# Kernel optimization log

Hardware: AMD Instinct MI355X
Metric: run time of the kernel (lower is better)

The kernel has to match this reference:

```python
import jax, jax.numpy as jnp
import numpy as np

B, S, D, H, E, K = 2, 1024, 512, 2048, 64, 2
EPS = 1e-5


def setup_inputs() -> dict:
    key = jax.random.key(0)
    ks = jax.random.split(key, 5)
    s = 0.02  # small init scale for stability
    return {
        "x": jax.random.normal(ks[0], (B, S, D), dtype=jnp.float32),
        "Wg": jax.random.normal(ks[1], (D, E), dtype=jnp.float32) * s,
        "bg": jnp.zeros((E,), dtype=jnp.float32),
        "W1": jax.random.normal(ks[2], (E, D, H), dtype=jnp.float32) * s,
        "b1": jnp.zeros((E, H), dtype=jnp.float32),
        "W2": jax.random.normal(ks[3], (E, H, D), dtype=jnp.float32) * s,
        "b2": jnp.zeros((E, D), dtype=jnp.float32),
        "gamma": jnp.ones((D,), dtype=jnp.float32),
        "beta": jnp.zeros((D,), dtype=jnp.float32),
    }


def reference(x, Wg, bg, W1, b1, W2, b2, gamma, beta):
    # Gating: softmax over experts, keep top-k weights, zero the rest (scatter)
    probs = jax.nn.softmax(x @ Wg + bg, axis=-1)          # [B,S,E]
    topk_vals, topk_idx = jax.lax.top_k(probs, K)          # [B,S,K]
    sparse_w = jnp.sum(
        jax.nn.one_hot(topk_idx, E, dtype=probs.dtype) * topk_vals[..., None],
        axis=-2,
    )                                                      # [B,S,E]

    # Dense MoE: run every expert FFN on every token (faithful to source)
    h = jax.nn.relu(jnp.einsum('bsd,edh->bseh', x, W1) + b1)   # [B,S,E,H]
    expert_out = jnp.einsum('bseh,ehd->bsed', h, W2) + b2      # [B,S,E,D]

    # Weighted combine + residual
    out = jnp.einsum('bse,bsed->bsd', sparse_w, expert_out) + x

    # LayerNorm (eps=1e-5, elementwise affine)
    mu = out.mean(-1, keepdims=True)
    var = ((out - mu) ** 2).mean(-1, keepdims=True)
    return (out - mu) * jax.lax.rsqrt(var + EPS) * gamma + beta
```

## Files before the change

### kernel.cpp

```cpp
#include <hip/hip_runtime.h>
#include <hip/hip_bf16.h>

#define NTOK 2048
#define DIM 512
#define HID 2048
#define NEXP 64
#define NSLICE 16
#define HSLICE 128
#define TTM 128
#define LN_EPS 1e-5f

#define WS_OFF 0
#define HS_OFF 10240
#define SMEM_BYTES 43008

typedef __bf16 bf16x8 __attribute__((ext_vector_type(8)));
typedef __bf16 bf16x4 __attribute__((ext_vector_type(4)));
typedef float f32x4 __attribute__((ext_vector_type(4)));

__global__ void init_kernel(float4* __restrict__ accb, int* __restrict__ counts) {
    int i = blockIdx.x * blockDim.x + threadIdx.x;
    accb[i] = make_float4(0.f, 0.f, 0.f, 0.f);
    if (i < NEXP) counts[i] = 0;
}

__global__ void gate_kernel(const float* __restrict__ x,
                            const float* __restrict__ Wg,
                            const float* __restrict__ bg,
                            int* __restrict__ counts,
                            int* __restrict__ btok,
                            float* __restrict__ bw) {
    const int t = blockIdx.x;
    const int lane = threadIdx.x;
    __shared__ float xs[DIM];
    const float4* xrow = (const float4*)(x + (size_t)t * DIM);
    ((float4*)xs)[lane] = xrow[lane];
    ((float4*)xs)[lane + 64] = xrow[lane + 64];
    __syncthreads();

    float acc = bg[lane];
    #pragma unroll 8
    for (int d = 0; d < DIM; d++) acc += xs[d] * Wg[d * NEXP + lane];

    float m = acc;
    #pragma unroll
    for (int off = 32; off; off >>= 1) m = fmaxf(m, __shfl_xor(m, off));
    float p = __expf(acc - m);
    float ssum = p;
    #pragma unroll
    for (int off = 32; off; off >>= 1) ssum += __shfl_xor(ssum, off);
    float prob = p / ssum;

    float v1 = prob; int i1 = lane;
    #pragma unroll
    for (int off = 32; off; off >>= 1) {
        float ov = __shfl_xor(v1, off);
        int   oi = __shfl_xor(i1, off);
        if (ov > v1 || (ov == v1 && oi < i1)) { v1 = ov; i1 = oi; }
    }
    float v2 = (lane == i1) ? -1e30f : prob; int i2 = lane;
    #pragma unroll
    for (int off = 32; off; off >>= 1) {
        float ov = __shfl_xor(v2, off);
        int   oi = __shfl_xor(i2, off);
        if (ov > v2 || (ov == v2 && oi < i2)) { v2 = ov; i2 = oi; }
    }

    if (lane == 0) {
        int s0 = atomicAdd(&counts[i1], 1);
        btok[i1 * NTOK + s0] = t;  bw[i1 * NTOK + s0] = v1;
        int s1 = atomicAdd(&counts[i2], 1);
        btok[i2 * NTOK + s1] = t;  bw[i2 * NTOK + s1] = v2;
    }
}

__device__ __forceinline__ int ws_off(int col, int kg) {
    return col * 40 + ((kg ^ ((col >> 3) & 3)) << 3);
}

__global__ __launch_bounds__(256, 3) void ffn_kernel(
    const float* __restrict__ x,
    const float* __restrict__ W1, const float* __restrict__ b1,
    const float* __restrict__ W2, const float* __restrict__ b2,
    const int* __restrict__ counts,
    const int* __restrict__ btok, const float* __restrict__ bw,
    float* __restrict__ accb)
{
    __shared__ char smem[SMEM_BYTES];
    __bf16* wsb = (__bf16*)(smem + WS_OFF);

    const int e = blockIdx.x >> 4;
    const int s = blockIdx.x & 15;
    const int n = counts[e];
    if (n <= 0) return;

    const int tid  = threadIdx.x;
    const int lane = tid & 63;
    const int wid  = tid >> 6;
    const int lq   = lane >> 4;
    const int lm   = lane & 15;
    const int c0   = (tid & 31) * 4;
    const int r0   = (tid >> 5) * 4;

    const float* W1s = W1 + (size_t)e * DIM * HID + s * HSLICE;
    const float* W2s = W2 + ((size_t)e * HID + (size_t)s * HSLICE) * DIM;
    const int*   btoke = btok + e * NTOK;
    const float* bwe   = bw   + e * NTOK;

    for (int t0 = 0; t0 < n; t0 += TTM) {
        const int tiln = min(TTM, n - t0);
        const bool two = (tiln > 64);

        const int tra0 = wid * 16 + lm;
        const int tok0 = btoke[t0 + (tra0 < tiln ? tra0 : 0)];
        const int tra1 = 64 + tra0;
        const int tok1 = two ? btoke[t0 + (tra1 < tiln ? tra1 : 0)] : tok0;
        const float* xrow0 = x + (size_t)tok0 * DIM;
        const float* xrow1 = x + (size_t)tok1 * DIM;

        f32x4 acc0[8], acc1[8];
        #pragma unroll
        for (int i = 0; i < 8; i++) { acc0[i] = (f32x4)0.0f; acc1[i] = (f32x4)0.0f; }

        for (int ks = 0; ks < 16; ks++) {
            float4 wv[4];
            const float* wp = W1s + (size_t)(ks * 32 + r0) * HID + c0;
            #pragma unroll
            for (int u = 0; u < 4; u++) wv[u] = *(const float4*)(wp + (size_t)u * HID);
            float4 a00 = *(const float4*)(xrow0 + ks * 32 + lq * 8);
            float4 a01 = *(const float4*)(xrow0 + ks * 32 + lq * 8 + 4);
            float4 a10, a11;
            if (two) {
                a10 = *(const float4*)(xrow1 + ks * 32 + lq * 8);
                a11 = *(const float4*)(xrow1 + ks * 32 + lq * 8 + 4);
            }

            __syncthreads();
            #pragma unroll
            for (int j = 0; j < 4; j++) {
                const float* f0 = (const float*)&wv[0];
                const float* f1 = (const float*)&wv[1];
                const float* f2 = (const float*)&wv[2];
                const float* f3 = (const float*)&wv[3];
                bf16x4 pk;
                pk[0] = (__bf16)f0[j]; pk[1] = (__bf16)f1[j];
                pk[2] = (__bf16)f2[j]; pk[3] = (__bf16)f3[j];
                *(bf16x4*)(wsb + ws_off(c0 + j, r0 >> 3) + (r0 & 7)) = pk;
            }
            bf16x8 af0, af1;
            {
                const float* f0 = (const float*)&a00;
                const float* f1 = (const float*)&a01;
                #pragma unroll
                for (int j = 0; j < 4; j++) { af0[j] = (__bf16)f0[j]; af0[4 + j] = (__bf16)f1[j]; }
            }
            if (two) {
                const float* f0 = (const float*)&a10;
                const float* f1 = (const float*)&a11;
                #pragma unroll
                for (int j = 0; j < 4; j++) { af1[j] = (__bf16)f0[j]; af1[4 + j] = (__bf16)f1[j]; }
            }
            __syncthreads();

            #pragma unroll
            for (int nt = 0; nt < 8; nt++) {
                bf16x8 bfv = *(const bf16x8*)(wsb + ws_off(nt * 16 + lm, lq));
                acc0[nt] = __builtin_amdgcn_mfma_f32_16x16x32_bf16(af0, bfv, acc0[nt], 0, 0, 0);
                if (two)
                    acc1[nt] = __builtin_amdgcn_mfma_f32_16x16x32_bf16(af1, bfv, acc1[nt], 0, 0, 0);
            }
        }

        #pragma unroll
        for (int nt = 0; nt < 8; nt++) {
            int hloc = nt * 16 + lm;
            float b1v = b1[e * HID + s * HSLICE + hloc];
            #pragma unroll
            for (int r = 0; r < 4; r++) {
                int tr = wid * 16 + lq * 4 + r;
                float v = fmaxf(acc0[nt][r] + b1v, 0.f);
                *(__bf16*)(smem + HS_OFF + tr * 256 +
                           (((hloc >> 3) ^ (tr & 7)) * 16) + (hloc & 7) * 2) = (__bf16)v;
                if (two) {
                    int tr1 = 64 + tr;
                    float v1 = fmaxf(acc1[nt][r] + b1v, 0.f);
                    *(__bf16*)(smem + HS_OFF + tr1 * 256 +
                               (((hloc >> 3) ^ (tr1 & 7)) * 16) + (hloc & 7) * 2) = (__bf16)v1;
                }
            }
        }

        for (int dq = 0; dq < 4; dq++) {
            f32x4 yacc0[8], yacc1[8];
            #pragma unroll
            for (int i = 0; i < 8; i++) { yacc0[i] = (f32x4)0.0f; yacc1[i] = (f32x4)0.0f; }

            for (int ks = 0; ks < 4; ks++) {
                float4 wv[4];
                const float* wp = W2s + (size_t)(ks * 32 + r0) * DIM + dq * 128 + c0;
                #pragma unroll
                for (int u = 0; u < 4; u++) wv[u] = *(const float4*)(wp + (size_t)u * DIM);

                const int trb0 = wid * 16 + lm;
                bf16x8 af0 = *(const bf16x8*)(smem + HS_OFF + trb0 * 256 +
                                              (((ks * 4 + lq) ^ (trb0 & 7)) * 16));
                bf16x8 af1;
                if (two) {
                    const int trb1 = 64 + trb0;
                    af1 = *(const bf16x8*)(smem + HS_OFF + trb1 * 256 +
                                           (((ks * 4 + lq) ^ (trb1 & 7)) * 16));
                }

                __syncthreads();
                #pragma unroll
                for (int j = 0; j < 4; j++) {
                    const float* f0 = (const float*)&wv[0];
                    const float* f1 = (const float*)&wv[1];
                    const float* f2 = (const float*)&wv[2];
                    const float* f3 = (const float*)&wv[3];
                    bf16x4 pk;
                    pk[0] = (__bf16)f0[j]; pk[1] = (__bf16)f1[j];
                    pk[2] = (__bf16)f2[j]; pk[3] = (__bf16)f3[j];
                    *(bf16x4*)(wsb + ws_off(c0 + j, r0 >> 3) + (r0 & 7)) = pk;
                }
                __syncthreads();

                #pragma unroll
                for (int nt = 0; nt < 8; nt++) {
                    bf16x8 bfv = *(const bf16x8*)(wsb + ws_off(nt * 16 + lm, lq));
                    yacc0[nt] = __builtin_amdgcn_mfma_f32_16x16x32_bf16(af0, bfv, yacc0[nt], 0, 0, 0);
                    if (two)
                        yacc1[nt] = __builtin_amdgcn_mfma_f32_16x16x32_bf16(af1, bfv, yacc1[nt], 0, 0, 0);
                }
            }

            float b2s[8];
            #pragma unroll
            for (int nt = 0; nt < 8; nt++) {
                int d = dq * 128 + nt * 16 + lm;
                b2s[nt] = (s == 0) ? b2[e * DIM + d] : 0.f;
            }
            #pragma unroll
            for (int r = 0; r < 4; r++) {
                int tr = wid * 16 + lq * 4 + r;
                if (tr < tiln) {
                    int tok2 = btoke[t0 + tr];
                    float w = bwe[t0 + tr];
                    float* dst = accb + (size_t)tok2 * DIM;
                    #pragma unroll
                    for (int nt = 0; nt < 8; nt++) {
                        int d = dq * 128 + nt * 16 + lm;
                        atomicAdd(dst + d, w * (yacc0[nt][r] + b2s[nt]));
                    }
                }
                if (two) {
                    int tr1 = 64 + tr;
                    if (tr1 < tiln) {
                        int tok2 = btoke[t0 + tr1];
                        float w = bwe[t0 + tr1];
                        float* dst = accb + (size_t)tok2 * DIM;
                        #pragma unroll
                        for (int nt = 0; nt < 8; nt++) {
                            int d = dq * 128 + nt * 16 + lm;
                            atomicAdd(dst + d, w * (yacc1[nt][r] + b2s[nt]));
                        }
                    }
                }
            }
        }
        __syncthreads();
    }
}

__global__ void ln_kernel(const float* __restrict__ x,
                          const float* __restrict__ accb,
                          const float* __restrict__ gamma,
                          const float* __restrict__ beta,
                          float* __restrict__ out) {
    const int t = blockIdx.x;
    const int tid = threadIdx.x;
    __shared__ float red[8];
    const size_t base = (size_t)t * DIM;
    float v0 = x[base + tid] + accb[base + tid];
    float v1 = x[base + 256 + tid] + accb[base + 256 + tid];
    float s  = v0 + v1;
    float sq = v0 * v0 + v1 * v1;
    #pragma unroll
    for (int off = 32; off; off >>= 1) { s += __shfl_xor(s, off); sq += __shfl_xor(sq, off); }
    if ((tid & 63) == 0) { red[tid >> 6] = s; red[4 + (tid >> 6)] = sq; }
    __syncthreads();
    float S  = red[0] + red[1] + red[2] + red[3];
    float SQ = red[4] + red[5] + red[6] + red[7];
    float mu  = S * (1.f / DIM);
    float var = SQ * (1.f / DIM) - mu * mu;
    float inv = rsqrtf(var + LN_EPS);
    out[base + tid]       = (v0 - mu) * inv * gamma[tid]       + beta[tid];
    out[base + 256 + tid] = (v1 - mu) * inv * gamma[256 + tid] + beta[256 + tid];
}

extern "C" void kernel_launch(void* const* d_in, const int* in_sizes, int n_in,
                              void* d_out, int out_size, void* d_ws, size_t ws_size,
                              hipStream_t stream) {
    const float* x     = (const float*)d_in[0];
    const float* Wg    = (const float*)d_in[1];
    const float* bg    = (const float*)d_in[2];
    const float* W1    = (const float*)d_in[3];
    const float* b1    = (const float*)d_in[4];
    const float* W2    = (const float*)d_in[5];
    const float* b2    = (const float*)d_in[6];
    const float* gamma = (const float*)d_in[7];
    const float* beta  = (const float*)d_in[8];

    char* ws = (char*)d_ws;
    int*   counts = (int*)ws;
    int*   btok   = (int*)(ws + 4096);
    float* bwv    = (float*)(ws + 4096 + 524288);
    float* accb   = (float*)(ws + 4096 + 2 * 524288);

    init_kernel<<<1024, 256, 0, stream>>>((float4*)accb, counts);
    gate_kernel<<<NTOK, 64, 0, stream>>>(x, Wg, bg, counts, btok, bwv);
    ffn_kernel<<<NEXP * NSLICE, 256, 0, stream>>>(x, W1, b1, W2, b2,
                                                  counts, btok, bwv, accb);
    ln_kernel<<<NTOK, 256, 0, stream>>>(x, accb, gamma, beta, (float*)d_out);
}
```

Measured before the change: 651.9 us.

## Double-buffer weight tiles in LDS and fold accumulator zeroing into gate kernel

Weight tiles for both FFN GEMMs are now prefetched into registers two steps ahead and stored into alternating LDS buffers, cutting per-step barriers from two to one and overlapping global loads with MFMA work. The W2 phase is flattened into a single 16-step loop to keep the pipeline running across output quarters. Zeroing of the accumulation buffer moves into the gate kernel, shrinking the init kernel to the counts reset. LDS use grows, which may lower occupancy.

Measured after the change: 763.4 us. 17.1% more time.

```diff
diff --git a/kernel.cpp b/kernel.cpp
--- a/kernel.cpp
+++ b/kernel.cpp
@@ -10,18 +10,22 @@
 #define TTM 128
 #define LN_EPS 1e-5f
 
-#define WS_OFF 0
-#define HS_OFF 10240
-#define SMEM_BYTES 43008
+#define WS0_OFF 0
+#define WS1_OFF 10240
+#define HS_OFF  20480
+#define SMEM_BYTES 53248
 
 typedef __bf16 bf16x8 __attribute__((ext_vector_type(8)));
 typedef __bf16 bf16x4 __attribute__((ext_vector_type(4)));
 typedef float f32x4 __attribute__((ext_vector_type(4)));
 
-__global__ void init_kernel(float4* __restrict__ accb, int* __restrict__ counts) {
-    int i = blockIdx.x * blockDim.x + threadIdx.x;
-    accb[i] = make_float4(0.f, 0.f, 0.f, 0.f);
-    if (i < NEXP) counts[i] = 0;
+#define LGKM_BARRIER() do { \
+    asm volatile("s_waitcnt lgkmcnt(0)" ::: "memory"); \
+    __builtin_amdgcn_s_barrier(); \
+} while (0)
+
+__global__ void init_kernel(int* __restrict__ counts) {
+    counts[threadIdx.x] = 0;
 }
 
 __global__ void gate_kernel(const float* __restrict__ x,
@@ -29,9 +33,14 @@
                             const float* __restrict__ bg,
                             int* __restrict__ counts,
                             int* __restrict__ btok,
-                            float* __restrict__ bw) {
+                            float* __restrict__ bw,
+                            float4* __restrict__ accb4) {
     const int t = blockIdx.x;
     const int lane = threadIdx.x;
+    const float4 z = make_float4(0.f, 0.f, 0.f, 0.f);
+    accb4[(size_t)t * (DIM / 4) + lane] = z;
+    accb4[(size_t)t * (DIM / 4) + lane + 64] = z;
+
     __shared__ float xs[DIM];
     const float4* xrow = (const float4*)(x + (size_t)t * DIM);
     ((float4*)xs)[lane] = xrow[lane];
@@ -76,6 +85,36 @@
 
 __device__ __forceinline__ int ws_off(int col, int kg) {
     return col * 40 + ((kg ^ ((col >> 3) & 3)) << 3);
+}
+
+__device__ __forceinline__ void wload(const float* __restrict__ wp, size_t rs,
+                                      float4 wv[4]) {
+    #pragma unroll
+    for (int u = 0; u < 4; u++) wv[u] = *(const float4*)(wp + (size_t)u * rs);
+}
+
+__device__ __forceinline__ void wstore(__bf16* __restrict__ wsb, int c0, int r0,
+                                       const float4 wv[4]) {
+    #pragma unroll
+    for (int j = 0; j < 4; j++) {
+        const float* f0 = (const float*)&wv[0];
+        const float* f1 = (const float*)&wv[1];
+        const float* f2 = (const float*)&wv[2];
+        const float* f3 = (const float*)&wv[3];
+        bf16x4 pk;
+        pk[0] = (__bf16)f0[j]; pk[1] = (__bf16)f1[j];
+        pk[2] = (__bf16)f2[j]; pk[3] = (__bf16)f3[j];
+        *(bf16x4*)(wsb + ws_off(c0 + j, r0 >> 3) + (r0 & 7)) = pk;
+    }
+}
+
+__device__ __forceinline__ bf16x8 acvt(float4 a0, float4 a1) {
+    bf16x8 v;
+    const float* f0 = (const float*)&a0;
+    const float* f1 = (const float*)&a1;
+    #pragma unroll
+    for (int j = 0; j < 4; j++) { v[j] = (__bf16)f0[j]; v[4 + j] = (__bf16)f1[j]; }
+    return v;
 }
 
 __global__ __launch_bounds__(256, 3) void ffn_kernel(
@@ -87,7 +126,8 @@
     float* __restrict__ accb)
 {
     __shared__ char smem[SMEM_BYTES];
-    __bf16* wsb = (__bf16*)(smem + WS_OFF);
+    __bf16* ws0 = (__bf16*)(smem + WS0_OFF);
+    __bf16* ws1 = (__bf16*)(smem + WS1_OFF);
 
     const int e = blockIdx.x >> 4;
     const int s = blockIdx.x & 15;
@@ -122,11 +162,17 @@
         #pragma unroll
         for (int i = 0; i < 8; i++) { acc0[i] = (f32x4)0.0f; acc1[i] = (f32x4)0.0f; }
 
+        float4 wv[4];
+        {
+            float4 w0[4];
+            wload(W1s + (size_t)r0 * HID + c0, HID, w0);
+            wstore(ws0, c0, r0, w0);
+            wload(W1s + (size_t)(32 + r0) * HID + c0, HID, wv);
+            LGKM_BARRIER();
+        }
+        int cur = 0;
+
         for (int ks = 0; ks < 16; ks++) {
-            float4 wv[4];
-            const float* wp = W1s + (size_t)(ks * 32 + r0) * HID + c0;
-            #pragma unroll
-            for (int u = 0; u < 4; u++) wv[u] = *(const float4*)(wp + (size_t)u * HID);
             float4 a00 = *(const float4*)(xrow0 + ks * 32 + lq * 8);
             float4 a01 = *(const float4*)(xrow0 + ks * 32 + lq * 8 + 4);
             float4 a10, a11;
@@ -134,40 +180,24 @@
                 a10 = *(const float4*)(xrow1 + ks * 32 + lq * 8);
                 a11 = *(const float4*)(xrow1 + ks * 32 + lq * 8 + 4);
             }
-
-            __syncthreads();
-            #pragma unroll
-            for (int j = 0; j < 4; j++) {
-                const float* f0 = (const float*)&wv[0];
-                const float* f1 = (const float*)&wv[1];
-                const float* f2 = (const float*)&wv[2];
-                const float* f3 = (const float*)&wv[3];
-                bf16x4 pk;
-                pk[0] = (__bf16)f0[j]; pk[1] = (__bf16)f1[j];
-                pk[2] = (__bf16)f2[j]; pk[3] = (__bf16)f3[j];
-                *(bf16x4*)(wsb + ws_off(c0 + j, r0 >> 3) + (r0 & 7)) = pk;
-            }
-            bf16x8 af0, af1;
-            {
-                const float* f0 = (const float*)&a00;
-                const float* f1 = (const float*)&a01;
-                #pragma unroll
-                for (int j = 0; j < 4; j++) { af0[j] = (__bf16)f0[j]; af0[4 + j] = (__bf16)f1[j]; }
-            }
-            if (two) {
-                const float* f0 = (const float*)&a10;
-                const float* f1 = (const float*)&a11;
-                #pragma unroll
-                for (int j = 0; j < 4; j++) { af1[j] = (__bf16)f0[j]; af1[4 + j] = (__bf16)f1[j]; }
-            }
-            __syncthreads();
-
+            bf16x8 af0 = acvt(a00, a01), af1;
+            if (two) af1 = acvt(a10, a11);
+
+            const __bf16* wr = cur ? ws1 : ws0;
             #pragma unroll
             for (int nt = 0; nt < 8; nt++) {
-                bf16x8 bfv = *(const bf16x8*)(wsb + ws_off(nt * 16 + lm, lq));
+                bf16x8 bfv = *(const bf16x8*)(wr + ws_off(nt * 16 + lm, lq));
                 acc0[nt] = __builtin_amdgcn_mfma_f32_16x16x32_bf16(af0, bfv, acc0[nt], 0, 0, 0);
                 if (two)
                     acc1[nt] = __builtin_amdgcn_mfma_f32_16x16x32_bf16(af1, bfv, acc1[nt], 0, 0, 0);
+            }
+            if (ks < 15) {
+                __bf16* ww = cur ? ws0 : ws1;
+                wstore(ww, c0, r0, wv);
+                if (ks < 14)
+                    wload(W1s + (size_t)((ks + 2) * 32 + r0) * HID + c0, HID, wv);
+                LGKM_BARRIER();
+                cur ^= 1;
             }
         }
 
@@ -190,85 +220,88 @@
             }
         }
 
-        for (int dq = 0; dq < 4; dq++) {
-            f32x4 yacc0[8], yacc1[8];
+        {
+            float4 w0[4];
+            wload(W2s + (size_t)r0 * DIM + c0, DIM, w0);
+            wstore(ws0, c0, r0, w0);
+            wload(W2s + (size_t)(32 + r0) * DIM + c0, DIM, wv);
+            LGKM_BARRIER();
+        }
+        cur = 0;
+        f32x4 yacc0[8], yacc1[8];
+
+        for (int u = 0; u < 16; u++) {
+            const int kk = u & 3, dq = u >> 2;
+            if (kk == 0) {
+                #pragma unroll
+                for (int i = 0; i < 8; i++) { yacc0[i] = (f32x4)0.0f; yacc1[i] = (f32x4)0.0f; }
+            }
+
+            const int trb0 = wid * 16 + lm;
+            bf16x8 af0 = *(const bf16x8*)(smem + HS_OFF + trb0 * 256 +
+                                          (((kk * 4 + lq) ^ (trb0 & 7)) * 16));
+            bf16x8 af1;
+            if (two) {
+                const int trb1 = 64 + trb0;
+                af1 = *(const bf16x8*)(smem + HS_OFF + trb1 * 256 +
+                                       (((kk * 4 + lq) ^ (trb1 & 7)) * 16));
+            }
+
+            const __bf16* wr = cur ? ws1 : ws0;
             #pragma unroll
-            for (int i = 0; i < 8; i++) { yacc0[i] = (f32x4)0.0f; yacc1[i] = (f32x4)0.0f; }
-
-            for (int ks = 0; ks < 4; ks++) {
-                float4 wv[4];
-                const float* wp = W2s + (size_t)(ks * 32 + r0) * DIM + dq * 128 + c0;
-                #pragma unroll
-                for (int u = 0; u < 4; u++) wv[u] = *(const float4*)(wp + (size_t)u * DIM);
-
-                const int trb0 = wid * 16 + lm;
-                bf16x8 af0 = *(const bf16x8*)(smem + HS_OFF + trb0 * 256 +
-                                              (((ks * 4 + lq) ^ (trb0 & 7)) * 16));
-                bf16x8 af1;
-                if (two) {
-                    const int trb1 = 64 + trb0;
-                    af1 = *(const bf16x8*)(smem + HS_OFF + trb1 * 256 +
-                                           (((ks * 4 + lq) ^ (trb1 & 7)) * 16));
+            for (int nt = 0; nt < 8; nt++) {
+                bf16x8 bfv = *(const bf16x8*)(wr + ws_off(nt * 16 + lm, lq));
+                yacc0[nt] = __builtin_amdgcn_mfma_f32_16x16x32_bf16(af0, bfv, yacc0[nt], 0, 0, 0);
+                if (two)
+                    yacc1[nt] = __builtin_amdgcn_mfma_f32_16x16x32_bf16(af1, bfv, yacc1[nt], 0, 0, 0);
+            }
+            if (u < 15) {
+                __bf16* ww = cur ? ws0 : ws1;
+                wstore(ww, c0, r0, wv);
+                if (u < 14) {
+                    const int un = u + 2;
+                    wload(W2s + (size_t)((un & 3) * 32 + r0) * DIM + (un >> 2) * 128 + c0,
+                          DIM, wv);
                 }
-
-                __syncthreads();
-                #pragma unroll
-                for (int j = 0; j < 4; j++) {
-                    const float* f0 = (const float*)&wv[0];
-                    const float* f1 = (const float*)&wv[1];
-                    const float* f2 = (const float*)&wv[2];
-                    const float* f3 = (const float*)&wv[3];
-                    bf16x4 pk;
-                    pk[0] = (__bf16)f0[j]; pk[1] = (__bf16)f1[j];
-                    pk[2] = (__bf16)f2[j]; pk[3] = (__bf16)f3[j];
-                    *(bf16x4*)(wsb + ws_off(c0 + j, r0 >> 3) + (r0 & 7)) = pk;
-                }
-                __syncthreads();
-
+                LGKM_BARRIER();
+                cur ^= 1;
+            }
+            if (kk == 3) {
+                float b2s[8];
                 #pragma unroll
                 for (int nt = 0; nt < 8; nt++) {
-                    bf16x8 bfv = *(const bf16x8*)(wsb + ws_off(nt * 16 + lm, lq));
-                    yacc0[nt] = __builtin_amdgcn_mfma_f32_16x16x32_bf16(af0, bfv, yacc0[nt], 0, 0, 0);
-                    if (two)
-                        yacc1[nt] = __builtin_amdgcn_mfma_f32_16x16x32_bf16(af1, bfv, yacc1[nt], 0, 0, 0);
+                    int d = dq * 128 + nt * 16 + lm;
+                    b2s[nt] = (s == 0) ? b2[e * DIM + d] : 0.f;
                 }
-            }
-
-            float b2s[8];
-            #pragma unroll
-            for (int nt = 0; nt < 8; nt++) {
-                int d = dq * 128 + nt * 16 + lm;
-                b2s[nt] = (s == 0) ? b2[e * DIM + d] : 0.f;
-            }
-            #pragma unroll
-            for (int r = 0; r < 4; r++) {
-                int tr = wid * 16 + lq * 4 + r;
-                if (tr < tiln) {
-                    int tok2 = btoke[t0 + tr];
-                    float w = bwe[t0 + tr];
-                    float* dst = accb + (size_t)tok2 * DIM;
-                    #pragma unroll
-                    for (int nt = 0; nt < 8; nt++) {
-                        int d = dq * 128 + nt * 16 + lm;
-                        atomicAdd(dst + d, w * (yacc0[nt][r] + b2s[nt]));
-                    }
-                }
-                if (two) {
-                    int tr1 = 64 + tr;
-                    if (tr1 < tiln) {
-                        int tok2 = btoke[t0 + tr1];
-                        float w = bwe[t0 + tr1];
+                #pragma unroll
+                for (int r = 0; r < 4; r++) {
+                    int tr = wid * 16 + lq * 4 + r;
+                    if (tr < tiln) {
+                        int tok2 = btoke[t0 + tr];
+                        float w = bwe[t0 + tr];
                         float* dst = accb + (size_t)tok2 * DIM;
                         #pragma unroll
                         for (int nt = 0; nt < 8; nt++) {
                             int d = dq * 128 + nt * 16 + lm;
-                            atomicAdd(dst + d, w * (yacc1[nt][r] + b2s[nt]));
+                            atomicAdd(dst + d, w * (yacc0[nt][r] + b2s[nt]));
+                        }
+                    }
+                    if (two) {
+                        int tr1 = 64 + tr;
+                        if (tr1 < tiln) {
+                            int tok2 = btoke[t0 + tr1];
+                            float w = bwe[t0 + tr1];
+                            float* dst = accb + (size_t)tok2 * DIM;
+                            #pragma unroll
+                            for (int nt = 0; nt < 8; nt++) {
+                                int d = dq * 128 + nt * 16 + lm;
+                                atomicAdd(dst + d, w * (yacc1[nt][r] + b2s[nt]));
+                            }
                         }
                     }
                 }
             }
         }
-        __syncthreads();
     }
 }
 
@@ -317,8 +350,9 @@
     float* bwv    = (float*)(ws + 4096 + 524288);
     float* accb   = (float*)(ws + 4096 + 2 * 524288);
 
-    init_kernel<<<1024, 256, 0, stream>>>((float4*)accb, counts);
-    gate_kernel<<<NTOK, 64, 0, stream>>>(x, Wg, bg, counts, btok, bwv);
+    init_kernel<<<1, NEXP, 0, stream>>>(counts);
+    gate_kernel<<<NTOK, 64, 0, stream>>>(x, Wg, bg, counts, btok, bwv,
+                                         (float4*)accb);
     ffn_kernel<<<NEXP * NSLICE, 256, 0, stream>>>(x, W1, b1, W2, b2,
                                                   counts, btok, bwv, accb);
     ln_kernel<<<NTOK, 256, 0, stream>>>(x, accb, gamma, beta, (float*)d_out);
```
